# Kernel tuning notes

Hardware: AMD Instinct MI355X
Metric: run time of the kernel (lower is better)

The kernel has to match this reference:

```python
import jax, jax.numpy as jnp
import numpy as np

BS, N, HEADS, DIN, DOUT = 512, 128, 8, 64, 64


def setup_inputs() -> dict:
    key = jax.random.key(0)
    k1, k2, k3, k4, k5 = jax.random.split(key, 5)
    h = jax.random.normal(k1, (BS, N, DIN), dtype=jnp.float32)
    w = jax.random.normal(k2, (HEADS, DIN, DOUT), dtype=jnp.float32) * 0.1
    a_src = jax.random.normal(k3, (HEADS, DOUT, 1), dtype=jnp.float32) * 0.1
    a_dst = jax.random.normal(k4, (HEADS, DOUT, 1), dtype=jnp.float32) * 0.1
    bias = jnp.zeros((DOUT,), dtype=jnp.float32)
    # sparse random adjacency with self-loops so every softmax row is valid
    adj = jax.random.uniform(k5, (BS, N, N)) < 0.05
    adj = adj | jnp.eye(N, dtype=bool)[None, :, :]
    return {"h": h, "adj": adj, "w": w, "a_src": a_src, "a_dst": a_dst, "bias": bias}


def reference(h, adj, w, a_src, a_dst, bias):
    # h: [b, n, i]; w: [H, i, o] -> h_prime: [b, H, n, o]
    h_prime = jnp.einsum('bni,hio->bhno', h, w)
    t = jnp.tanh(h_prime)
    attn_src = jnp.einsum('bhno,ho->bhn', t, a_src[..., 0])  # [b, H, n]
    attn_dst = jnp.einsum('bhno,ho->bhn', t, a_dst[..., 0])  # [b, H, n]
    # attn[b,h,i,j] = src[b,h,i] + dst[b,h,j]
    attn = attn_src[..., :, None] + attn_dst[..., None, :]
    attn = jax.nn.leaky_relu(attn, negative_slope=0.2)
    attn = jnp.where(adj[:, None, :, :], attn, -jnp.inf)
    attn = jax.nn.softmax(attn, axis=-1)
    out = jnp.einsum('bhij,bhjo->bhio', attn, h_prime)
    return out + bias
```

## Files before the change

### kernel.cpp

```cpp
#include <hip/hip_runtime.h>

#define BSZ 512
#define NN 128
#define HEADS 8
#define DIN 64
#define DOUT 64

typedef __bf16 bf16x8 __attribute__((ext_vector_type(8)));
typedef float floatx4 __attribute__((ext_vector_type(4)));

static __device__ __forceinline__ unsigned short f2bf(float f) {
    __bf16 b = (__bf16)f;
    return __builtin_bit_cast(unsigned short, b);
}
static __device__ __forceinline__ bf16x8 ld_frag(const unsigned short* p) {
    uint4 r = *reinterpret_cast<const uint4*>(p);
    return __builtin_bit_cast(bf16x8, r);
}

__global__ __launch_bounds__(512, 4) void gat_fwd(
    const float* __restrict__ hin,
    const int*   __restrict__ adj,
    const float* __restrict__ w,
    const float* __restrict__ a_src,
    const float* __restrict__ a_dst,
    const float* __restrict__ bias,
    float* __restrict__ out)
{
    __shared__ __attribute__((aligned(16))) unsigned short wT[DOUT * DIN];
    __shared__ __attribute__((aligned(16))) unsigned short hpT[DOUT * NN];
    __shared__ __attribute__((aligned(16))) unsigned short P[NN * NN];
    __shared__ __attribute__((aligned(16))) unsigned int   msk[NN * 4];
    __shared__ __attribute__((aligned(16))) float s_src[NN];
    __shared__ __attribute__((aligned(16))) float s_dst[NN];

    const int b    = blockIdx.x;
    const int tid  = threadIdx.x;
    const int lane = tid & 63;
    const int wv   = tid >> 6;
    const int lg   = lane >> 4;
    const int lm   = lane & 15;
    const int n0   = wv * 16;

    const float* hb = hin + (size_t)b * NN * DIN;
    bf16x8 hA[2];
    #pragma unroll
    for (int kt = 0; kt < 2; ++kt) {
        const float* p = hb + (n0 + lm) * DIN + kt * 32 + lg * 8;
        float4 v0 = *reinterpret_cast<const float4*>(p);
        float4 v1 = *reinterpret_cast<const float4*>(p + 4);
        bf16x8 a;
        a[0] = (__bf16)v0.x; a[1] = (__bf16)v0.y; a[2] = (__bf16)v0.z; a[3] = (__bf16)v0.w;
        a[4] = (__bf16)v1.x; a[5] = (__bf16)v1.y; a[6] = (__bf16)v1.z; a[7] = (__bf16)v1.w;
        hA[kt] = a;
    }

    const int* adjb = adj + (size_t)b * NN * NN;
    for (int it = 0; it < 32; ++it) {
        const int idx = wv * 2048 + it * 64 + lane;
        unsigned long long m = __ballot(adjb[idx] != 0);
        if (lane == 0) {
            const int row = idx >> 7, half = (idx >> 6) & 1;
            msk[row * 4 + half * 2]     = (unsigned int)m;
            msk[row * 4 + half * 2 + 1] = (unsigned int)(m >> 32);
        }
    }
    auto stage_w = [&](int hd) {
        const float* wg = w + hd * DIN * DOUT;
        const int o = tid & 63, kb = (tid >> 6) * 8;
        unsigned int u[4];
        #pragma unroll
        for (int p = 0; p < 4; ++p) {
            float f0 = wg[(kb + 2 * p) * DOUT + o];
            float f1 = wg[(kb + 2 * p + 1) * DOUT + o];
            u[p] = f2bf(f0) | ((unsigned int)f2bf(f1) << 16);
        }
        const int idx = (o * 64 + kb) ^ ((o & 7) << 3);
        *reinterpret_cast<uint4*>(&wT[idx]) = make_uint4(u[0], u[1], u[2], u[3]);
    };
    stage_w(0);
    __syncthreads();

    float* outb = out + (size_t)b * HEADS * NN * DOUT;
    float bo[4];
    #pragma unroll
    for (int nt = 0; nt < 4; ++nt) bo[nt] = bias[nt * 16 + lm];

    for (int hd = 0; hd < HEADS; ++hd) {
        floatx4 acc[4] = {floatx4{0,0,0,0}, floatx4{0,0,0,0}, floatx4{0,0,0,0}, floatx4{0,0,0,0}};
        #pragma unroll
        for (int kt = 0; kt < 2; ++kt) {
            #pragma unroll
            for (int nt = 0; nt < 4; ++nt) {
                const int o = nt * 16 + lm;
                bf16x8 bfr = ld_frag(&wT[(o * 64 + kt * 32 + lg * 8) ^ ((o & 7) << 3)]);
                acc[nt] = __builtin_amdgcn_mfma_f32_16x16x32_bf16(hA[kt], bfr, acc[nt], 0, 0, 0);
            }
        }
        const float* asp = a_src + hd * DOUT;
        const float* adp = a_dst + hd * DOUT;
        float ps[4] = {0, 0, 0, 0}, pd[4] = {0, 0, 0, 0};
        #pragma unroll
        for (int nt = 0; nt < 4; ++nt) {
            const int o = nt * 16 + lm;
            const float as = asp[o], ad = adp[o];
            #pragma unroll
            for (int r = 0; r < 4; ++r) {
                const float v = acc[nt][r];
                const float ex = __expf(2.f * v);
                const float t = 1.f - 2.f / (ex + 1.f);
                ps[r] = fmaf(t, as, ps[r]);
                pd[r] = fmaf(t, ad, pd[r]);
            }
            const int jb = n0 + lg * 4;
            unsigned int u01 = f2bf(acc[nt][0]) | ((unsigned int)f2bf(acc[nt][1]) << 16);
            unsigned int u23 = f2bf(acc[nt][2]) | ((unsigned int)f2bf(acc[nt][3]) << 16);
            const int base = (o * 128 + jb) ^ ((o & 7) << 3);
            *reinterpret_cast<unsigned int*>(&hpT[base])     = u01;
            *reinterpret_cast<unsigned int*>(&hpT[base + 2]) = u23;
        }
        #pragma unroll
        for (int r = 0; r < 4; ++r) {
            #pragma unroll
            for (int m = 1; m <= 8; m <<= 1) {
                ps[r] += __shfl_xor(ps[r], m);
                pd[r] += __shfl_xor(pd[r], m);
            }
        }
        if (lm == 0) {
            #pragma unroll
            for (int r = 0; r < 4; ++r) {
                s_src[n0 + lg * 4 + r] = ps[r];
                s_dst[n0 + lg * 4 + r] = pd[r];
            }
        }
        __syncthreads();

        if (hd + 1 < HEADS) stage_w(hd + 1);

        const int i = n0 + lm;
        const int sw = (i & 7) << 3;
        const float si = s_src[i];

        const int pz = i * 128 + lg * 32;
        #pragma unroll
        for (int t = 0; t < 4; ++t)
            *reinterpret_cast<uint4*>(&P[(pz + 8 * t) ^ sw]) = make_uint4(0, 0, 0, 0);

        unsigned int m = msk[i * 4 + lg];
        float sum = 0.f;
        while (m) {
            const int q = __builtin_ctz(m); m &= m - 1;
            const float x = si + s_dst[lg * 32 + q];
            const float xl = fmaxf(x, 0.f) + 0.2f * fminf(x, 0.f);
            const float e = __expf(xl);
            const __bf16 eb = (__bf16)e;
            sum += (float)eb;
            P[(pz + q) ^ sw] = __builtin_bit_cast(unsigned short, eb);
        }
        sum += __shfl_xor(sum, 16);
        sum += __shfl_xor(sum, 32);
        const float inv = 1.f / sum;

        floatx4 oacc[4] = {floatx4{0,0,0,0}, floatx4{0,0,0,0}, floatx4{0,0,0,0}, floatx4{0,0,0,0}};
        #pragma unroll
        for (int kt = 0; kt < 4; ++kt) {
            const bf16x8 af = ld_frag(&P[(i * 128 + kt * 32 + lg * 8) ^ sw]);
            #pragma unroll
            for (int nt = 0; nt < 4; ++nt) {
                const int o = nt * 16 + lm;
                bf16x8 bfr = ld_frag(&hpT[(o * 128 + kt * 32 + lg * 8) ^ ((o & 7) << 3)]);
                oacc[nt] = __builtin_amdgcn_mfma_f32_16x16x32_bf16(af, bfr, oacc[nt], 0, 0, 0);
            }
        }
        float invr[4];
        #pragma unroll
        for (int r = 0; r < 4; ++r) invr[r] = __shfl(inv, lg * 4 + r);
        #pragma unroll
        for (int nt = 0; nt < 4; ++nt) {
            const int o = nt * 16 + lm;
            #pragma unroll
            for (int r = 0; r < 4; ++r) {
                const int row = n0 + lg * 4 + r;
                outb[(size_t)hd * NN * DOUT + row * DOUT + o] = fmaf(oacc[nt][r], invr[r], bo[nt]);
            }
        }
        __syncthreads();
    }
}

extern "C" void kernel_launch(void* const* d_in, const int* in_sizes, int n_in,
                              void* d_out, int out_size, void* d_ws, size_t ws_size,
                              hipStream_t stream) {
    (void)in_sizes; (void)n_in; (void)out_size; (void)d_ws; (void)ws_size;
    const float* h     = (const float*)d_in[0];
    const int*   adj   = (const int*)d_in[1];
    const float* w     = (const float*)d_in[2];
    const float* a_src = (const float*)d_in[3];
    const float* a_dst = (const float*)d_in[4];
    const float* bias  = (const float*)d_in[5];
    float* out = (float*)d_out;
    gat_fwd<<<dim3(BSZ), dim3(512), 0, stream>>>(h, adj, w, a_src, a_dst, bias, out);
}
```

Before: 66.94 us.

## Split GAT kernel across heads with one block per batch-head pair

Launches one block per (batch, head) instead of looping over eight heads inside one block per batch, so the grid grows eightfold and head iterations with their barriers run in parallel across CUs. Weights are now read straight from global memory into MFMA fragments instead of staged through LDS, and the adjacency mask is built from vectorized int4 loads rather than a ballot loop. In exchange, each block reloads h and the full adjacency matrix for its batch, multiplying that global traffic by the head count, and the weight reads become strided scalar loads.

```diff
diff --git a/kernel.cpp b/kernel.cpp
--- a/kernel.cpp
+++ b/kernel.cpp
@@ -18,7 +18,7 @@
     return __builtin_bit_cast(bf16x8, r);
 }
 
-__global__ __launch_bounds__(512, 4) void gat_fwd(
+__global__ __launch_bounds__(512, 6) void gat_fwd(
     const float* __restrict__ hin,
     const int*   __restrict__ adj,
     const float* __restrict__ w,
@@ -27,14 +27,15 @@
     const float* __restrict__ bias,
     float* __restrict__ out)
 {
-    __shared__ __attribute__((aligned(16))) unsigned short wT[DOUT * DIN];
     __shared__ __attribute__((aligned(16))) unsigned short hpT[DOUT * NN];
     __shared__ __attribute__((aligned(16))) unsigned short P[NN * NN];
     __shared__ __attribute__((aligned(16))) unsigned int   msk[NN * 4];
     __shared__ __attribute__((aligned(16))) float s_src[NN];
     __shared__ __attribute__((aligned(16))) float s_dst[NN];
 
-    const int b    = blockIdx.x;
+    const int bid  = blockIdx.x;
+    const int hd   = bid >> 9;
+    const int b    = bid & 511;
     const int tid  = threadIdx.x;
     const int lane = tid & 63;
     const int wv   = tid >> 6;
@@ -55,137 +56,123 @@
         hA[kt] = a;
     }
 
-    const int* adjb = adj + (size_t)b * NN * NN;
-    for (int it = 0; it < 32; ++it) {
-        const int idx = wv * 2048 + it * 64 + lane;
-        unsigned long long m = __ballot(adjb[idx] != 0);
-        if (lane == 0) {
-            const int row = idx >> 7, half = (idx >> 6) & 1;
-            msk[row * 4 + half * 2]     = (unsigned int)m;
-            msk[row * 4 + half * 2 + 1] = (unsigned int)(m >> 32);
+    {
+        const int row = n0 + (lane >> 2);
+        const int wd  = lane & 3;
+        const int* ap = adj + (size_t)b * NN * NN + row * NN + wd * 32;
+        unsigned int m = 0;
+        #pragma unroll
+        for (int t = 0; t < 8; ++t) {
+            int4 v = *reinterpret_cast<const int4*>(ap + t * 4);
+            m |= (v.x != 0 ? (1u << (4 * t + 0)) : 0u)
+               | (v.y != 0 ? (1u << (4 * t + 1)) : 0u)
+               | (v.z != 0 ? (1u << (4 * t + 2)) : 0u)
+               | (v.w != 0 ? (1u << (4 * t + 3)) : 0u);
+        }
+        msk[row * 4 + wd] = m;
+    }
+
+    const float* wg = w + hd * DIN * DOUT;
+    floatx4 acc[4] = {floatx4{0,0,0,0}, floatx4{0,0,0,0}, floatx4{0,0,0,0}, floatx4{0,0,0,0}};
+    #pragma unroll
+    for (int kt = 0; kt < 2; ++kt) {
+        #pragma unroll
+        for (int nt = 0; nt < 4; ++nt) {
+            const float* wp = wg + (kt * 32 + lg * 8) * DOUT + nt * 16 + lm;
+            bf16x8 bfr;
+            #pragma unroll
+            for (int q = 0; q < 8; ++q) bfr[q] = (__bf16)wp[q * DOUT];
+            acc[nt] = __builtin_amdgcn_mfma_f32_16x16x32_bf16(hA[kt], bfr, acc[nt], 0, 0, 0);
         }
     }
-    auto stage_w = [&](int hd) {
-        const float* wg = w + hd * DIN * DOUT;
-        const int o = tid & 63, kb = (tid >> 6) * 8;
-        unsigned int u[4];
+    const float* asp = a_src + hd * DOUT;
+    const float* adp = a_dst + hd * DOUT;
+    float ps[4] = {0, 0, 0, 0}, pd[4] = {0, 0, 0, 0};
+    #pragma unroll
+    for (int nt = 0; nt < 4; ++nt) {
+        const int o = nt * 16 + lm;
+        const float as = asp[o], ad = adp[o];
         #pragma unroll
-        for (int p = 0; p < 4; ++p) {
-            float f0 = wg[(kb + 2 * p) * DOUT + o];
-            float f1 = wg[(kb + 2 * p + 1) * DOUT + o];
-            u[p] = f2bf(f0) | ((unsigned int)f2bf(f1) << 16);
+        for (int r = 0; r < 4; ++r) {
+            const float v = acc[nt][r];
+            const float ex = __expf(2.f * v);
+            const float t = 1.f - 2.f / (ex + 1.f);
+            ps[r] = fmaf(t, as, ps[r]);
+            pd[r] = fmaf(t, ad, pd[r]);
         }
-        const int idx = (o * 64 + kb) ^ ((o & 7) << 3);
-        *reinterpret_cast<uint4*>(&wT[idx]) = make_uint4(u[0], u[1], u[2], u[3]);
-    };
-    stage_w(0);
+        const int jb = n0 + lg * 4;
+        unsigned int u01 = f2bf(acc[nt][0]) | ((unsigned int)f2bf(acc[nt][1]) << 16);
+        unsigned int u23 = f2bf(acc[nt][2]) | ((unsigned int)f2bf(acc[nt][3]) << 16);
+        const int base = (o * 128 + jb) ^ ((o & 7) << 3);
+        *reinterpret_cast<unsigned int*>(&hpT[base])     = u01;
+        *reinterpret_cast<unsigned int*>(&hpT[base + 2]) = u23;
+    }
+    #pragma unroll
+    for (int r = 0; r < 4; ++r) {
+        #pragma unroll
+        for (int m = 1; m <= 8; m <<= 1) {
+            ps[r] += __shfl_xor(ps[r], m);
+            pd[r] += __shfl_xor(pd[r], m);
+        }
+    }
+    if (lm == 0) {
+        #pragma unroll
+        for (int r = 0; r < 4; ++r) {
+            s_src[n0 + lg * 4 + r] = ps[r];
+            s_dst[n0 + lg * 4 + r] = pd[r];
+        }
+    }
     __syncthreads();
 
-    float* outb = out + (size_t)b * HEADS * NN * DOUT;
-    float bo[4];
+    const int i = n0 + lm;
+    const int sw = (i & 7) << 3;
+    const float si = s_src[i];
+
+    const int pz = i * 128 + lg * 32;
     #pragma unroll
-    for (int nt = 0; nt < 4; ++nt) bo[nt] = bias[nt * 16 + lm];
+    for (int t = 0; t < 4; ++t)
+        *reinterpret_cast<uint4*>(&P[(pz + 8 * t) ^ sw]) = make_uint4(0, 0, 0, 0);
 
-    for (int hd = 0; hd < HEADS; ++hd) {
-        floatx4 acc[4] = {floatx4{0,0,0,0}, floatx4{0,0,0,0}, floatx4{0,0,0,0}, floatx4{0,0,0,0}};
-        #pragma unroll
-        for (int kt = 0; kt < 2; ++kt) {
-            #pragma unroll
-            for (int nt = 0; nt < 4; ++nt) {
-                const int o = nt * 16 + lm;
-                bf16x8 bfr = ld_frag(&wT[(o * 64 + kt * 32 + lg * 8) ^ ((o & 7) << 3)]);
-                acc[nt] = __builtin_amdgcn_mfma_f32_16x16x32_bf16(hA[kt], bfr, acc[nt], 0, 0, 0);
-            }
-        }
-        const float* asp = a_src + hd * DOUT;
-        const float* adp = a_dst + hd * DOUT;
-        float ps[4] = {0, 0, 0, 0}, pd[4] = {0, 0, 0, 0};
+    unsigned int m = msk[i * 4 + lg];
+    float sum = 0.f;
+    while (m) {
+        const int q = __builtin_ctz(m); m &= m - 1;
+        const float x = si + s_dst[lg * 32 + q];
+        const float xl = fmaxf(x, 0.f) + 0.2f * fminf(x, 0.f);
+        const float e = __expf(xl);
+        const __bf16 eb = (__bf16)e;
+        sum += (float)eb;
+        P[(pz + q) ^ sw] = __builtin_bit_cast(unsigned short, eb);
+    }
+    sum += __shfl_xor(sum, 16);
+    sum += __shfl_xor(sum, 32);
+    const float inv = 1.f / sum;
+
+    floatx4 oacc[4] = {floatx4{0,0,0,0}, floatx4{0,0,0,0}, floatx4{0,0,0,0}, floatx4{0,0,0,0}};
+    #pragma unroll
+    for (int kt = 0; kt < 4; ++kt) {
+        const bf16x8 af = ld_frag(&P[(i * 128 + kt * 32 + lg * 8) ^ sw]);
         #pragma unroll
         for (int nt = 0; nt < 4; ++nt) {
             const int o = nt * 16 + lm;
-            const float as = asp[o], ad = adp[o];
-            #pragma unroll
-            for (int r = 0; r < 4; ++r) {
-                const float v = acc[nt][r];
-                const float ex = __expf(2.f * v);
-                const float t = 1.f - 2.f / (ex + 1.f);
-                ps[r] = fmaf(t, as, ps[r]);
-                pd[r] = fmaf(t, ad, pd[r]);
-            }
-            const int jb = n0 + lg * 4;
-            unsigned int u01 = f2bf(acc[nt][0]) | ((unsigned int)f2bf(acc[nt][1]) << 16);
-            unsigned int u23 = f2bf(acc[nt][2]) | ((unsigned int)f2bf(acc[nt][3]) << 16);
-            const int base = (o * 128 + jb) ^ ((o & 7) << 3);
-            *reinterpret_cast<unsigned int*>(&hpT[base])     = u01;
-            *reinterpret_cast<unsigned int*>(&hpT[base + 2]) = u23;
+            bf16x8 bfr = ld_frag(&hpT[(o * 128 + kt * 32 + lg * 8) ^ ((o & 7) << 3)]);
+            oacc[nt] = __builtin_amdgcn_mfma_f32_16x16x32_bf16(af, bfr, oacc[nt], 0, 0, 0);
         }
+    }
+    float invr[4];
+    #pragma unroll
+    for (int r = 0; r < 4; ++r) invr[r] = __shfl(inv, lg * 4 + r);
+
+    float* outb = out + ((size_t)b * HEADS + hd) * NN * DOUT;
+    #pragma unroll
+    for (int nt = 0; nt < 4; ++nt) {
+        const int o = nt * 16 + lm;
+        const float bo = bias[o];
         #pragma unroll
         for (int r = 0; r < 4; ++r) {
-            #pragma unroll
-            for (int m = 1; m <= 8; m <<= 1) {
-                ps[r] += __shfl_xor(ps[r], m);
-                pd[r] += __shfl_xor(pd[r], m);
-            }
+            const int row = n0 + lg * 4 + r;
+            outb[row * DOUT + o] = fmaf(oacc[nt][r], invr[r], bo);
         }
-        if (lm == 0) {
-            #pragma unroll
-            for (int r = 0; r < 4; ++r) {
-                s_src[n0 + lg * 4 + r] = ps[r];
-                s_dst[n0 + lg * 4 + r] = pd[r];
-            }
-        }
-        __syncthreads();
-
-        if (hd + 1 < HEADS) stage_w(hd + 1);
-
-        const int i = n0 + lm;
-        const int sw = (i & 7) << 3;
-        const float si = s_src[i];
-
-        const int pz = i * 128 + lg * 32;
-        #pragma unroll
-        for (int t = 0; t < 4; ++t)
-            *reinterpret_cast<uint4*>(&P[(pz + 8 * t) ^ sw]) = make_uint4(0, 0, 0, 0);
-
-        unsigned int m = msk[i * 4 + lg];
-        float sum = 0.f;
-        while (m) {
-            const int q = __builtin_ctz(m); m &= m - 1;
-            const float x = si + s_dst[lg * 32 + q];
-            const float xl = fmaxf(x, 0.f) + 0.2f * fminf(x, 0.f);
-            const float e = __expf(xl);
-            const __bf16 eb = (__bf16)e;
-            sum += (float)eb;
-            P[(pz + q) ^ sw] = __builtin_bit_cast(unsigned short, eb);
-        }
-        sum += __shfl_xor(sum, 16);
-        sum += __shfl_xor(sum, 32);
-        const float inv = 1.f / sum;
-
-        floatx4 oacc[4] = {floatx4{0,0,0,0}, floatx4{0,0,0,0}, floatx4{0,0,0,0}, floatx4{0,0,0,0}};
-        #pragma unroll
-        for (int kt = 0; kt < 4; ++kt) {
-            const bf16x8 af = ld_frag(&P[(i * 128 + kt * 32 + lg * 8) ^ sw]);
-            #pragma unroll
-            for (int nt = 0; nt < 4; ++nt) {
-                const int o = nt * 16 + lm;
-                bf16x8 bfr = ld_frag(&hpT[(o * 128 + kt * 32 + lg * 8) ^ ((o & 7) << 3)]);
-                oacc[nt] = __builtin_amdgcn_mfma_f32_16x16x32_bf16(af, bfr, oacc[nt], 0, 0, 0);
-            }
-        }
-        float invr[4];
-        #pragma unroll
-        for (int r = 0; r < 4; ++r) invr[r] = __shfl(inv, lg * 4 + r);
-        #pragma unroll
-        for (int nt = 0; nt < 4; ++nt) {
-            const int o = nt * 16 + lm;
-            #pragma unroll
-            for (int r = 0; r < 4; ++r) {
-                const int row = n0 + lg * 4 + r;
-                outb[(size_t)hd * NN * DOUT + row * DOUT + o] = fmaf(oacc[nt][r], invr[r], bo[nt]);
-            }
-        }
-        __syncthreads();
     }
 }
 
@@ -200,5 +187,5 @@
     const float* a_dst = (const float*)d_in[4];
     const float* bias  = (const float*)d_in[5];
     float* out = (float*)d_out;
-    gat_fwd<<<dim3(BSZ), dim3(512), 0, stream>>>(h, adj, w, a_src, a_dst, bias, out);
+    gat_fwd<<<dim3(BSZ * HEADS), dim3(512), 0, stream>>>(h, adj, w, a_src, a_dst, bias, out);
 }
```

Measured after the change: 89.33 us. +33.5%, slower.
